# Kernel optimization log

Measured on AMD Instinct MI355X. Metric: run time of the kernel, lower is better.

## Reference

```python
import jax, jax.numpy as jnp
import numpy as np

B, S, H, D = 4, 2048, 12, 64
HIDDEN = H * D  # 768
WINDOW = 64     # config.local_attention // 2
ROPE_THETA = 10000.0  # local_rope_theta for sliding layers


def rotate_half(x):
    d = x.shape[-1] // 2
    return jnp.concatenate([-x[..., d:], x[..., :d]], axis=-1)


def setup_inputs() -> dict:
    key = jax.random.key(0)
    k1, k2, k3 = jax.random.split(key, 3)
    hidden_states = jax.random.normal(k1, (B, S, HIDDEN), dtype=jnp.float32)
    # RoPE tables (HF style): inv_freq over half dims, duplicated
    inv_freq = 1.0 / (ROPE_THETA ** (jnp.arange(0, D, 2, dtype=jnp.float32) / D))  # [D/2]
    pos = jnp.arange(S, dtype=jnp.float32)
    freqs = pos[:, None] * inv_freq[None, :]          # [S, D/2]
    emb = jnp.concatenate([freqs, freqs], axis=-1)    # [S, D]
    cos = jnp.broadcast_to(jnp.cos(emb)[None], (B, S, D))
    sin = jnp.broadcast_to(jnp.sin(emb)[None], (B, S, D))
    # sliding-window additive mask [B,1,S,S]
    idx = jnp.arange(S)
    allowed = jnp.abs(idx[:, None] - idx[None, :]) <= WINDOW
    neg = jnp.finfo(jnp.float32).min
    attention_mask = jnp.broadcast_to(
        jnp.where(allowed, 0.0, neg)[None, None], (B, 1, S, S)
    ).astype(jnp.float32)
    std = 0.02
    Wqkv_w = jax.random.normal(k2, (3 * HIDDEN, HIDDEN), dtype=jnp.float32) * std
    Wo_w = jax.random.normal(k3, (HIDDEN, HIDDEN), dtype=jnp.float32) * std
    return {"hidden_states": hidden_states, "cos": cos, "sin": sin,
            "attention_mask": attention_mask, "Wqkv_w": Wqkv_w, "Wo_w": Wo_w}


def reference(hidden_states, cos, sin, attention_mask, Wqkv_w, Wo_w):
    b, s, _ = hidden_states.shape
    scaling = D ** -0.5
    qkv = hidden_states @ Wqkv_w.T                       # [B,S,3*HIDDEN]
    qkv = qkv.reshape(b, s, 3, H, D)
    q = jnp.transpose(qkv[:, :, 0], (0, 2, 1, 3))        # [B,H,S,D]
    k = jnp.transpose(qkv[:, :, 1], (0, 2, 1, 3))
    v = jnp.transpose(qkv[:, :, 2], (0, 2, 1, 3))
    # RoPE with float32 intermediates (inputs already fp32 here)
    c = cos[:, None].astype(jnp.float32)                 # [B,1,S,D]
    sn = sin[:, None].astype(jnp.float32)
    qf, kf = q.astype(jnp.float32), k.astype(jnp.float32)
    q = (qf * c + rotate_half(qf) * sn).astype(q.dtype)
    k = (kf * c + rotate_half(kf) * sn).astype(k.dtype)
    # SDPA with explicit additive mask
    scores = jnp.einsum('bhqd,bhkd->bhqk', q, k) * scaling + attention_mask
    attn = jax.nn.softmax(scores, axis=-1)
    out = jnp.einsum('bhqk,bhkd->bhqd', attn, v)         # [B,H,S,D]
    out = jnp.transpose(out, (0, 2, 1, 3)).reshape(b, s, HIDDEN)
    return out @ Wo_w.T
```

## Files before the change

### kernel.cpp

```cpp
#include <hip/hip_runtime.h>
#include <math.h>


typedef __attribute__((ext_vector_type(8))) short short8;
typedef __attribute__((ext_vector_type(4))) float floatx4;

constexpr int kB = 4;
constexpr int kS = 2048;
constexpr int kH = 12;
constexpr int kD = 64;
constexpr int kHidden = 768;
constexpr int kQKV = 3 * kHidden;

__device__ __forceinline__ unsigned short f2bf(float f) {
  union { float f; unsigned int u; } x; x.f = f;
  unsigned int r = (x.u + 0x7fffu + ((x.u >> 16) & 1u)) >> 16;
  return (unsigned short)r;
}

__global__ __launch_bounds__(256) void cvt_all(
    const float* __restrict__ h, const float* __restrict__ wqkv,
    const float* __restrict__ wo, unsigned short* __restrict__ hb,
    unsigned short* __restrict__ wqb, unsigned short* __restrict__ wob) {
  constexpr int n1 = kB * kS * kHidden / 4;
  constexpr int n2 = kQKV * kHidden / 4;
  constexpr int n3 = kHidden * kHidden / 4;
  int i = blockIdx.x * 256 + threadIdx.x;
  const float* src;
  unsigned short* dst;
  if (i < n1) {
    src = h; dst = hb;
  } else if (i < n1 + n2) {
    i -= n1; src = wqkv; dst = wqb;
  } else {
    i -= n1 + n2; if (i >= n3) return; src = wo; dst = wob;
  }
  const float4 v = ((const float4*)src)[i];
  ushort4 o;
  o.x = f2bf(v.x); o.y = f2bf(v.y); o.z = f2bf(v.z); o.w = f2bf(v.w);
  ((ushort4*)dst)[i] = o;
}

__device__ __forceinline__ void gload_lds16(const unsigned short* g, unsigned short* l) {
  __builtin_amdgcn_global_load_lds(
      (const __attribute__((address_space(1))) unsigned int*)g,
      (__attribute__((address_space(3))) unsigned int*)l, 16, 0, 0);
}

__global__ __launch_bounds__(512) void gemm_qkv(
    const unsigned short* __restrict__ A,
    const unsigned short* __restrict__ B,
    const float* __restrict__ cosp, const float* __restrict__ sinp,
    unsigned short* __restrict__ Qr, unsigned short* __restrict__ Kr,
    unsigned short* __restrict__ Vt) {
  constexpr int K = kHidden;
  __shared__ unsigned short SH[128 * 136];
  unsigned short* As = SH;
  unsigned short* Bs = SH + 128 * 64;

  const int tid = threadIdx.x;
  const int lane = tid & 63;
  const int wave = tid >> 6;
  const int m0 = blockIdx.x * 128;
  const int n0 = blockIdx.y * 128;

  int ldsS[2];
  const unsigned short* gA[2];
  const unsigned short* gB[2];
#pragma unroll
  for (int t = 0; t < 2; t++) {
    const int ci = (wave * 2 + t) * 64 + lane;
    const int row = ci >> 3;
    const int c = (ci & 7) ^ (row & 7);
    ldsS[t] = ci * 8;
    gA[t] = A + (size_t)(m0 + row) * K + c * 8;
    gB[t] = B + (size_t)(n0 + row) * K + c * 8;
  }

  const int wm = wave >> 1, wn = wave & 1;
  const int mr = wm * 32 + (lane & 15);
  const int nr = wn * 64 + (lane & 15);
  const int kq = lane >> 4;

  floatx4 acc[2][4];
#pragma unroll
  for (int i = 0; i < 2; i++)
#pragma unroll
    for (int j = 0; j < 4; j++) acc[i][j] = (floatx4)(0.f);

  for (int k0 = 0; k0 < K; k0 += 64) {
    if (k0) __syncthreads();
#pragma unroll
    for (int t = 0; t < 2; t++) {
      gload_lds16(gA[t] + k0, &As[ldsS[t]]);
      gload_lds16(gB[t] + k0, &Bs[ldsS[t]]);
    }
    __syncthreads();
#pragma unroll
    for (int s = 0; s < 2; s++) {
      short8 af[2], bf[4];
#pragma unroll
      for (int i = 0; i < 2; i++)
        af[i] = *(const short8*)&As[(mr + i * 16) * 64 + (((s * 4 + kq) ^ (mr & 7)) * 8)];
#pragma unroll
      for (int j = 0; j < 4; j++)
        bf[j] = *(const short8*)&Bs[(nr + j * 16) * 64 + (((s * 4 + kq) ^ (nr & 7)) * 8)];
#pragma unroll
      for (int i = 0; i < 2; i++)
#pragma unroll
        for (int j = 0; j < 4; j++)
          acc[i][j] = __builtin_amdgcn_mfma_f32_16x16x32_bf16(af[i], bf[j],
                                                              acc[i][j], 0, 0, 0);
    }
  }

  __syncthreads();
  unsigned short (*Obuf)[136] = (unsigned short (*)[136])SH;

  const int region = n0 / kHidden;
  const int b = m0 >> 11, s0 = m0 & 2047;
  const int h0 = (n0 % kHidden) >> 6;
  const int rowL0 = wm * 32 + kq * 4;

  if (region == 2) {
#pragma unroll
    for (int i = 0; i < 2; i++)
#pragma unroll
      for (int r = 0; r < 4; r++) {
        const int rowL = rowL0 + i * 16 + r;
#pragma unroll
        for (int j = 0; j < 4; j++)
          Obuf[wn * 64 + j * 16 + (lane & 15)][rowL] = f2bf(acc[i][j][r]);
      }
    __syncthreads();
#pragma unroll
    for (int it = 0; it < 4; it++) {
      const int t = tid + it * 512;
      const int s8 = t & 15, rowc = t >> 4;
      const int hl = rowc >> 6, d = rowc & 63;
      *(short8*)(Vt + ((size_t)(b * kH + h0 + hl) * kD + d) * kS + s0 + s8 * 8) =
          *(const short8*)&Obuf[rowc][s8 * 8];
    }
  } else {
    unsigned short* dst = (region == 0) ? Qr : Kr;
    const float qscale = (region == 0) ? 0.125f : 1.f;
#pragma unroll
    for (int i = 0; i < 2; i++)
#pragma unroll
      for (int r = 0; r < 4; r++) {
        const int rowL = rowL0 + i * 16 + r;
        const int s = s0 + rowL;
        const float* cs = cosp + ((size_t)(b * kS + s)) * kD;
        const float* sns = sinp + ((size_t)(b * kS + s)) * kD;
#pragma unroll
        for (int jp = 0; jp < 2; jp++) {
          const int colL = wn * 64 + jp * 16 + (lane & 15);
          const int d = colL & 63;
          const float c = cs[d], sn = sns[d];
          const float xlo = acc[i][jp][r], xhi = acc[i][jp + 2][r];
          Obuf[rowL][colL]      = f2bf((xlo * c - xhi * sn) * qscale);
          Obuf[rowL][colL + 32] = f2bf((xhi * c + xlo * sn) * qscale);
        }
      }
    __syncthreads();
#pragma unroll
    for (int it = 0; it < 4; it++) {
      const int t = tid + it * 512;
      const int d8 = t & 7, sl = (t >> 3) & 127, hl = t >> 10;
      *(short8*)(dst + ((size_t)(b * kH + h0 + hl) * kS + s0 + sl) * kD + d8 * 8) =
          *(const short8*)&Obuf[sl][hl * 64 + d8 * 8];
    }
  }
}

__global__ __launch_bounds__(512) void gemm_bf16_nt(
    const unsigned short* __restrict__ A, const unsigned short* __restrict__ B,
    float* __restrict__ C, int M, int N, int K) {
  __shared__ unsigned short As[128 * 64];
  __shared__ unsigned short Bs[128 * 64];

  const int tid = threadIdx.x;
  const int lane = tid & 63;
  const int wave = tid >> 6;
  const int m0 = blockIdx.x * 128;
  const int n0 = blockIdx.y * 128;

  int ldsS[2];
  const unsigned short* gA[2];
  const unsigned short* gB[2];
#pragma unroll
  for (int t = 0; t < 2; t++) {
    const int ci = (wave * 2 + t) * 64 + lane;
    const int row = ci >> 3;
    const int c = (ci & 7) ^ (row & 7);
    ldsS[t] = ci * 8;
    gA[t] = A + (size_t)(m0 + row) * K + c * 8;
    gB[t] = B + (size_t)(n0 + row) * K + c * 8;
  }

  const int wm = wave >> 1, wn = wave & 1;
  const int mr = wm * 32 + (lane & 15);
  const int nr = wn * 64 + (lane & 15);
  const int kq = lane >> 4;

  floatx4 acc[2][4];
#pragma unroll
  for (int i = 0; i < 2; i++)
#pragma unroll
    for (int j = 0; j < 4; j++) acc[i][j] = (floatx4)(0.f);

  for (int k0 = 0; k0 < K; k0 += 64) {
    if (k0) __syncthreads();
#pragma unroll
    for (int t = 0; t < 2; t++) {
      gload_lds16(gA[t] + k0, &As[ldsS[t]]);
      gload_lds16(gB[t] + k0, &Bs[ldsS[t]]);
    }
    __syncthreads();
#pragma unroll
    for (int s = 0; s < 2; s++) {
      short8 af[2], bf[4];
#pragma unroll
      for (int i = 0; i < 2; i++)
        af[i] = *(const short8*)&As[(mr + i * 16) * 64 + (((s * 4 + kq) ^ (mr & 7)) * 8)];
#pragma unroll
      for (int j = 0; j < 4; j++)
        bf[j] = *(const short8*)&Bs[(nr + j * 16) * 64 + (((s * 4 + kq) ^ (nr & 7)) * 8)];
#pragma unroll
      for (int i = 0; i < 2; i++)
#pragma unroll
        for (int j = 0; j < 4; j++)
          acc[i][j] = __builtin_amdgcn_mfma_f32_16x16x32_bf16(af[i], bf[j],
                                                              acc[i][j], 0, 0, 0);
    }
  }

  const int crow = m0 + wm * 32 + kq * 4;
  const int ccol = n0 + wn * 64 + (lane & 15);
#pragma unroll
  for (int i = 0; i < 2; i++)
#pragma unroll
    for (int r = 0; r < 4; r++) {
      float* cp = C + (size_t)(crow + i * 16 + r) * N + ccol;
#pragma unroll
      for (int j = 0; j < 4; j++) cp[j * 16] = acc[i][j][r];
    }
}

constexpr int AQT = 32;

__global__ __launch_bounds__(256) void attn_v3(
    const unsigned short* __restrict__ Qr, const unsigned short* __restrict__ Kr,
    const unsigned short* __restrict__ Vt, unsigned short* __restrict__ out) {
  __shared__ unsigned short Pfrag[2][5][64][8];
  __shared__ float Ssum[2][AQT];

  const int tid = threadIdx.x;
  const int lane = tid & 63;
  const int wave = tid >> 6;
  const int quad = lane >> 4;
  const int l15 = lane & 15;
  const int qbase = blockIdx.x * AQT;
  const int h = blockIdx.y, b = blockIdx.z;
  const int bh = b * kH + h;
  const int kbase = qbase - 64;
  const int tq = wave >> 1;
  const int kh = wave & 1;

  short8 vf[2][5];
  {
    const unsigned short* vbase = Vt + (size_t)bh * kD * kS;
#pragma unroll
    for (int nt = 0; nt < 2; nt++) {
      const unsigned short* vrow = vbase + (size_t)(kh * 32 + nt * 16 + l15) * kS;
#pragma unroll
      for (int kk = 0; kk < 5; kk++) {
        int s0 = kbase + kk * 32 + quad * 8;
        s0 = min(max(s0, 0), kS - 8);
        vf[nt][kk] = *(const short8*)(vrow + s0);
      }
    }
  }

  const unsigned short* qsrc =
      Qr + ((size_t)bh * kS + qbase + tq * 16 + l15) * kD + quad * 8;
  const short8 a0 = *(const short8*)qsrc;
  const short8 a1 = *(const short8*)(qsrc + 32);

  floatx4 acc[5];
  const unsigned short* ksrc = Kr + (size_t)bh * kS * kD;
#pragma unroll
  for (int g = 0; g < 5; g++) {
    int row = kbase + (kh * 5 + g) * 16 + l15;
    row = min(max(row, 0), kS - 1);
    const unsigned short* kp = ksrc + (size_t)row * kD + quad * 8;
    const short8 b0 = *(const short8*)kp;
    const short8 b1 = *(const short8*)(kp + 32);
    floatx4 z = (floatx4)(0.f);
    z = __builtin_amdgcn_mfma_f32_16x16x32_bf16(a0, b0, z, 0, 0, 0);
    z = __builtin_amdgcn_mfma_f32_16x16x32_bf16(a1, b1, z, 0, 0, 0);
    acc[g] = z;
  }

#pragma unroll
  for (int r = 0; r < 4; r++) {
    const int q = tq * 16 + quad * 4 + r;
    float s = 0.f;
#pragma unroll
    for (int g = 0; g < 5; g++) {
      const int key = (kh * 5 + g) * 16 + l15;
      const int kg_ = kbase + key;
      const bool valid = (key >= q) && (key <= q + 128) && (kg_ >= 0) && (kg_ < kS);
      const float e = valid ? __expf(acc[g][r]) : 0.f;
      s += e;
      Pfrag[tq][key >> 5][((key >> 3) & 3) * 16 + quad * 4 + r][key & 7] = f2bf(e);
    }
#pragma unroll
    for (int off = 1; off < 16; off <<= 1) s += __shfl_xor(s, off, 64);
    if (l15 == 0) Ssum[kh][q] = s;
  }
  __syncthreads();

  floatx4 o0 = (floatx4)(0.f), o1 = (floatx4)(0.f);
#pragma unroll
  for (int kk = 0; kk < 5; kk++) {
    const short8 pa = *(const short8*)&Pfrag[tq][kk][lane][0];
    o0 = __builtin_amdgcn_mfma_f32_16x16x32_bf16(pa, vf[0][kk], o0, 0, 0, 0);
    o1 = __builtin_amdgcn_mfma_f32_16x16x32_bf16(pa, vf[1][kk], o1, 0, 0, 0);
  }

#pragma unroll
  for (int r = 0; r < 4; r++) {
    const int q = tq * 16 + quad * 4 + r;
    const float inv = 1.f / (Ssum[0][q] + Ssum[1][q]);
    unsigned short* op =
        out + ((size_t)(b * kS + qbase + q)) * kHidden + h * kD + kh * 32 + l15;
    op[0] = f2bf(o0[r] * inv);
    op[16] = f2bf(o1[r] * inv);
  }
}

extern "C" void kernel_launch(void* const* d_in, const int* in_sizes, int n_in,
                              void* d_out, int out_size, void* d_ws,
                              size_t ws_size, hipStream_t stream) {
  const float* hidden = (const float*)d_in[0];
  const float* cosp = (const float*)d_in[1];
  const float* sinp = (const float*)d_in[2];
  const float* wqkv = (const float*)d_in[4];
  const float* wo = (const float*)d_in[5];
  float* out = (float*)d_out;

  const int M = kB * kS;
  const size_t szH = (size_t)M * kHidden;

  unsigned short* hbf = (unsigned short*)d_ws;
  unsigned short* wqkvbf = hbf + szH;
  unsigned short* wobf = wqkvbf + (size_t)kQKV * kHidden;
  unsigned short* attnbf = wobf + (size_t)kHidden * kHidden;
  unsigned short* Qrb = attnbf + szH;
  unsigned short* Krb = Qrb + szH;
  unsigned short* Vtb = Krb + szH;

  const int ncvt = (M * kHidden + kQKV * kHidden + kHidden * kHidden) / 4;
  cvt_all<<<(ncvt + 255) / 256, 256, 0, stream>>>(hidden, wqkv, wo, hbf,
                                                  wqkvbf, wobf);

  dim3 g1(M / 128, kQKV / 128);
  gemm_qkv<<<g1, 512, 0, stream>>>(hbf, wqkvbf, cosp, sinp, Qrb, Krb, Vtb);

  dim3 ga(kS / AQT, kH, kB);
  attn_v3<<<ga, 256, 0, stream>>>(Qrb, Krb, Vtb, attnbf);

  dim3 g2(M / 128, kHidden / 128);
  gemm_bf16_nt<<<g2, 512, 0, stream>>>(attnbf, wobf, out, M, kHidden, kHidden);
}
```

Baseline: 218.4 us.

## Double-buffer GEMM K-loop with half-tile prefetch; use 4-wave 64x64 tiles for output GEMM

Both GEMM kernels now split each 64-wide K step into two 32-wide halves held in ping-pong LDS buffers. Loads for the next half are issued before computing the current one, with explicit vmcnt waits and raw s_barrier, so global-to-LDS transfers overlap with MFMA work. A new XOR swizzle suits the 32-column layout. The output projection GEMM also drops from 8 waves to 4, each wave computing a 64x64 tile with more accumulators. That raises register use and may lower occupancy, and the hand-written waitcnt/barrier ordering is fragile.

```diff
diff --git a/kernel.cpp b/kernel.cpp
--- a/kernel.cpp
+++ b/kernel.cpp
@@ -54,9 +54,12 @@
     unsigned short* __restrict__ Qr, unsigned short* __restrict__ Kr,
     unsigned short* __restrict__ Vt) {
   constexpr int K = kHidden;
+  constexpr int NP = 2 * (K / 64);
   __shared__ unsigned short SH[128 * 136];
-  unsigned short* As = SH;
-  unsigned short* Bs = SH + 128 * 64;
+  unsigned short* Ah0 = SH;
+  unsigned short* Ah1 = SH + 4096;
+  unsigned short* Bh0 = SH + 8192;
+  unsigned short* Bh1 = SH + 12288;
 
   const int tid = threadIdx.x;
   const int lane = tid & 63;
@@ -64,57 +67,69 @@
   const int m0 = blockIdx.x * 128;
   const int n0 = blockIdx.y * 128;
 
-  int ldsS[2];
-  const unsigned short* gA[2];
-  const unsigned short* gB[2];
-#pragma unroll
-  for (int t = 0; t < 2; t++) {
-    const int ci = (wave * 2 + t) * 64 + lane;
-    const int row = ci >> 3;
-    const int c = (ci & 7) ^ (row & 7);
-    ldsS[t] = ci * 8;
-    gA[t] = A + (size_t)(m0 + row) * K + c * 8;
-    gB[t] = B + (size_t)(n0 + row) * K + c * 8;
-  }
+  const int sc = wave * 64 + lane;
+  const int srow = sc >> 2;
+  const int sgc = ((sc & 3) ^ ((srow >> 1) & 3)) * 8;
+  const int ldsOff = sc * 8;
+  const unsigned short* gA0 = A + (size_t)(m0 + srow) * K + sgc;
+  const unsigned short* gB0 = B + (size_t)(n0 + srow) * K + sgc;
 
   const int wm = wave >> 1, wn = wave & 1;
   const int mr = wm * 32 + (lane & 15);
   const int nr = wn * 64 + (lane & 15);
   const int kq = lane >> 4;
 
+  int aOff[2], bOff[4];
+#pragma unroll
+  for (int i = 0; i < 2; i++) {
+    const int r = mr + i * 16;
+    aOff[i] = (r * 4 + (kq ^ ((r >> 1) & 3))) * 8;
+  }
+#pragma unroll
+  for (int j = 0; j < 4; j++) {
+    const int r = nr + j * 16;
+    bOff[j] = (r * 4 + (kq ^ ((r >> 1) & 3))) * 8;
+  }
+
   floatx4 acc[2][4];
 #pragma unroll
   for (int i = 0; i < 2; i++)
 #pragma unroll
     for (int j = 0; j < 4; j++) acc[i][j] = (floatx4)(0.f);
 
-  for (int k0 = 0; k0 < K; k0 += 64) {
-    if (k0) __syncthreads();
-#pragma unroll
-    for (int t = 0; t < 2; t++) {
-      gload_lds16(gA[t] + k0, &As[ldsS[t]]);
-      gload_lds16(gB[t] + k0, &Bs[ldsS[t]]);
-    }
-    __syncthreads();
-#pragma unroll
-    for (int s = 0; s < 2; s++) {
-      short8 af[2], bf[4];
-#pragma unroll
-      for (int i = 0; i < 2; i++)
-        af[i] = *(const short8*)&As[(mr + i * 16) * 64 + (((s * 4 + kq) ^ (mr & 7)) * 8)];
+  gload_lds16(gA0, &Ah0[ldsOff]);
+  gload_lds16(gB0, &Bh0[ldsOff]);
+
+  for (int p = 0; p < NP; ++p) {
+    if (p + 1 < NP) {
+      const int kn = ((p + 1) >> 1) * 64 + ((p + 1) & 1) * 32;
+      unsigned short* Ad = ((p + 1) & 1) ? Ah1 : Ah0;
+      unsigned short* Bd = ((p + 1) & 1) ? Bh1 : Bh0;
+      gload_lds16(gA0 + kn, &Ad[ldsOff]);
+      gload_lds16(gB0 + kn, &Bd[ldsOff]);
+      asm volatile("s_waitcnt vmcnt(2)" ::: "memory");
+    } else {
+      asm volatile("s_waitcnt vmcnt(0)" ::: "memory");
+    }
+    __builtin_amdgcn_s_barrier();
+    __builtin_amdgcn_sched_barrier(0);
+    const unsigned short* Asb = (p & 1) ? Ah1 : Ah0;
+    const unsigned short* Bsb = (p & 1) ? Bh1 : Bh0;
+    short8 af[2], bf[4];
+#pragma unroll
+    for (int i = 0; i < 2; i++) af[i] = *(const short8*)&Asb[aOff[i]];
+#pragma unroll
+    for (int j = 0; j < 4; j++) bf[j] = *(const short8*)&Bsb[bOff[j]];
+#pragma unroll
+    for (int i = 0; i < 2; i++)
 #pragma unroll
       for (int j = 0; j < 4; j++)
-        bf[j] = *(const short8*)&Bs[(nr + j * 16) * 64 + (((s * 4 + kq) ^ (nr & 7)) * 8)];
-#pragma unroll
-      for (int i = 0; i < 2; i++)
-#pragma unroll
-        for (int j = 0; j < 4; j++)
-          acc[i][j] = __builtin_amdgcn_mfma_f32_16x16x32_bf16(af[i], bf[j],
-                                                              acc[i][j], 0, 0, 0);
-    }
-  }
-
-  __syncthreads();
+        acc[i][j] = __builtin_amdgcn_mfma_f32_16x16x32_bf16(af[i], bf[j],
+                                                            acc[i][j], 0, 0, 0);
+    __builtin_amdgcn_sched_barrier(0);
+    __builtin_amdgcn_s_barrier();
+  }
+
   unsigned short (*Obuf)[136] = (unsigned short (*)[136])SH;
 
   const int region = n0 / kHidden;
@@ -173,72 +188,99 @@
   }
 }
 
-__global__ __launch_bounds__(512) void gemm_bf16_nt(
+__global__ __launch_bounds__(256) void gemm_bf16_nt(
     const unsigned short* __restrict__ A, const unsigned short* __restrict__ B,
     float* __restrict__ C, int M, int N, int K) {
-  __shared__ unsigned short As[128 * 64];
-  __shared__ unsigned short Bs[128 * 64];
+  __shared__ unsigned short SH[4 * 4096];
+  unsigned short* Ah0 = SH;
+  unsigned short* Ah1 = SH + 4096;
+  unsigned short* Bh0 = SH + 8192;
+  unsigned short* Bh1 = SH + 12288;
 
   const int tid = threadIdx.x;
   const int lane = tid & 63;
   const int wave = tid >> 6;
   const int m0 = blockIdx.x * 128;
   const int n0 = blockIdx.y * 128;
-
-  int ldsS[2];
-  const unsigned short* gA[2];
-  const unsigned short* gB[2];
+  const int NP = 2 * (K / 64);
+
+  int ldsOff[2];
+  const unsigned short* gA0[2];
+  const unsigned short* gB0[2];
 #pragma unroll
   for (int t = 0; t < 2; t++) {
-    const int ci = (wave * 2 + t) * 64 + lane;
-    const int row = ci >> 3;
-    const int c = (ci & 7) ^ (row & 7);
-    ldsS[t] = ci * 8;
-    gA[t] = A + (size_t)(m0 + row) * K + c * 8;
-    gB[t] = B + (size_t)(n0 + row) * K + c * 8;
+    const int sc = wave * 128 + t * 64 + lane;
+    const int srow = sc >> 2;
+    const int sgc = ((sc & 3) ^ ((srow >> 1) & 3)) * 8;
+    ldsOff[t] = sc * 8;
+    gA0[t] = A + (size_t)(m0 + srow) * K + sgc;
+    gB0[t] = B + (size_t)(n0 + srow) * K + sgc;
   }
 
   const int wm = wave >> 1, wn = wave & 1;
-  const int mr = wm * 32 + (lane & 15);
+  const int mr = wm * 64 + (lane & 15);
   const int nr = wn * 64 + (lane & 15);
   const int kq = lane >> 4;
 
-  floatx4 acc[2][4];
-#pragma unroll
-  for (int i = 0; i < 2; i++)
+  int aOff[4], bOff[4];
+#pragma unroll
+  for (int i = 0; i < 4; i++) {
+    const int ra = mr + i * 16;
+    aOff[i] = (ra * 4 + (kq ^ ((ra >> 1) & 3))) * 8;
+    const int rb = nr + i * 16;
+    bOff[i] = (rb * 4 + (kq ^ ((rb >> 1) & 3))) * 8;
+  }
+
+  floatx4 acc[4][4];
+#pragma unroll
+  for (int i = 0; i < 4; i++)
 #pragma unroll
     for (int j = 0; j < 4; j++) acc[i][j] = (floatx4)(0.f);
 
-  for (int k0 = 0; k0 < K; k0 += 64) {
-    if (k0) __syncthreads();
-#pragma unroll
-    for (int t = 0; t < 2; t++) {
-      gload_lds16(gA[t] + k0, &As[ldsS[t]]);
-      gload_lds16(gB[t] + k0, &Bs[ldsS[t]]);
-    }
-    __syncthreads();
-#pragma unroll
-    for (int s = 0; s < 2; s++) {
-      short8 af[2], bf[4];
-#pragma unroll
-      for (int i = 0; i < 2; i++)
-        af[i] = *(const short8*)&As[(mr + i * 16) * 64 + (((s * 4 + kq) ^ (mr & 7)) * 8)];
+#pragma unroll
+  for (int t = 0; t < 2; t++) {
+    gload_lds16(gA0[t], &Ah0[ldsOff[t]]);
+    gload_lds16(gB0[t], &Bh0[ldsOff[t]]);
+  }
+
+  for (int p = 0; p < NP; ++p) {
+    if (p + 1 < NP) {
+      const int kn = ((p + 1) >> 1) * 64 + ((p + 1) & 1) * 32;
+      unsigned short* Ad = ((p + 1) & 1) ? Ah1 : Ah0;
+      unsigned short* Bd = ((p + 1) & 1) ? Bh1 : Bh0;
+#pragma unroll
+      for (int t = 0; t < 2; t++) {
+        gload_lds16(gA0[t] + kn, &Ad[ldsOff[t]]);
+        gload_lds16(gB0[t] + kn, &Bd[ldsOff[t]]);
+      }
+      asm volatile("s_waitcnt vmcnt(4)" ::: "memory");
+    } else {
+      asm volatile("s_waitcnt vmcnt(0)" ::: "memory");
+    }
+    __builtin_amdgcn_s_barrier();
+    __builtin_amdgcn_sched_barrier(0);
+    const unsigned short* Asb = (p & 1) ? Ah1 : Ah0;
+    const unsigned short* Bsb = (p & 1) ? Bh1 : Bh0;
+    short8 af[4], bf[4];
+#pragma unroll
+    for (int i = 0; i < 4; i++) {
+      af[i] = *(const short8*)&Asb[aOff[i]];
+      bf[i] = *(const short8*)&Bsb[bOff[i]];
+    }
+#pragma unroll
+    for (int i = 0; i < 4; i++)
 #pragma unroll
       for (int j = 0; j < 4; j++)
-        bf[j] = *(const short8*)&Bs[(nr + j * 16) * 64 + (((s * 4 + kq) ^ (nr & 7)) * 8)];
-#pragma unroll
-      for (int i = 0; i < 2; i++)
-#pragma unroll
-        for (int j = 0; j < 4; j++)
-          acc[i][j] = __builtin_amdgcn_mfma_f32_16x16x32_bf16(af[i], bf[j],
-                                                              acc[i][j], 0, 0, 0);
-    }
-  }
-
-  const int crow = m0 + wm * 32 + kq * 4;
+        acc[i][j] = __builtin_amdgcn_mfma_f32_16x16x32_bf16(af[i], bf[j],
+                                                            acc[i][j], 0, 0, 0);
+    __builtin_amdgcn_sched_barrier(0);
+    __builtin_amdgcn_s_barrier();
+  }
+
+  const int crow = m0 + wm * 64 + kq * 4;
   const int ccol = n0 + wn * 64 + (lane & 15);
 #pragma unroll
-  for (int i = 0; i < 2; i++)
+  for (int i = 0; i < 4; i++)
 #pragma unroll
     for (int r = 0; r < 4; r++) {
       float* cp = C + (size_t)(crow + i * 16 + r) * N + ccol;
@@ -372,5 +414,5 @@
   attn_v3<<<ga, 256, 0, stream>>>(Qrb, Krb, Vtb, attnbf);
 
   dim3 g2(M / 128, kHidden / 128);
-  gemm_bf16_nt<<<g2, 512, 0, stream>>>(attnbf, wobf, out, M, kHidden, kHidden);
-}
+  gemm_bf16_nt<<<g2, 256, 0, stream>>>(attnbf, wobf, out, M, kHidden, kHidden);
+}
```

Result: no change. 215.3 us (-1.4%).
